# Kernel tuning notes

Hardware: AMD Instinct MI355X
Metric: run time of the kernel (lower is better)

The kernel has to match this reference:

```python
import jax, jax.numpy as jnp
import numpy as np

B_, T_, D_ = 4, 4096, 512
H_, DH_ = 8, 64
N_HASHES, BUCKET = 4, 64
SELF_ATTN_VAL = -5e4  # TOKEN_SELF_ATTN_VALUE from reformer-pytorch


def setup_inputs() -> dict:
    key = jax.random.key(0)
    ks = jax.random.split(key, 12)
    s = 0.02
    return {
        "src": jax.random.normal(ks[0], (B_, T_, D_), jnp.float32),
        "Wqk": jax.random.normal(ks[1], (D_, D_), jnp.float32) * s,
        "Wv": jax.random.normal(ks[2], (D_, D_), jnp.float32) * s,
        "Wout": jax.random.normal(ks[3], (D_, D_), jnp.float32) * s,
        "bout": jnp.zeros((D_,), jnp.float32),
        "W1": jax.random.normal(ks[4], (D_, 2048), jnp.float32) * s,
        "b1": jnp.zeros((2048,), jnp.float32),
        "W2": jax.random.normal(ks[5], (2048, D_), jnp.float32) * s,
        "b2": jnp.zeros((D_,), jnp.float32),
        "gamma": jnp.ones((D_,), jnp.float32),
        "beta": jnp.zeros((D_,), jnp.float32),
        "rotations": jax.random.normal(ks[6], (DH_, N_HASHES, (T_ // BUCKET) // 2), jnp.float32),
    }


def _look_one_back(x):
    # concat each chunk with the previous chunk (wraparound), along the slot axis
    prev = jnp.concatenate([x[:, -1:], x[:, :-1]], axis=1)
    return jnp.concatenate([x, prev], axis=2)


def lsh_attention(qk, v, rotations):
    # qk, v: (B, T, d) with B = batch*heads; shared-QK LSH attention (non-causal,
    # attend_across_buckets=True, allow_duplicate_attention=True, no dropout)
    B, T, d = qk.shape
    n_buckets = T // BUCKET
    # --- hashing ---
    rv = jnp.einsum("btf,fhi->bhti", qk, rotations)          # (B, n_hashes, T, nb/2)
    rv = jnp.concatenate([rv, -rv], axis=-1)                  # (B, n_hashes, T, nb)
    buckets = jnp.argmax(rv, axis=-1)                         # (B, n_hashes, T)
    offsets = (jnp.arange(N_HASHES) * n_buckets)[None, :, None]
    buckets = (buckets + offsets).reshape(B, N_HASHES * T)
    # --- sort by (bucket, position) ---
    ticker = jnp.arange(N_HASHES * T)
    buckets_and_t = buckets * T + (ticker % T)[None, :]
    sticker = jnp.argsort(buckets_and_t, axis=-1)             # (B, n_hashes*T)
    undo_sort = jnp.argsort(sticker, axis=-1)
    st = sticker % T
    sqk = jnp.take_along_axis(qk, st[..., None], axis=1)      # (B, n_hashes*T, d)
    sv = jnp.take_along_axis(v, st[..., None], axis=1)
    # --- chunk ---
    chunks = N_HASHES * n_buckets
    bq_t = st.reshape(B, chunks, BUCKET)
    bqk = sqk.reshape(B, chunks, BUCKET, d)
    bv = sv.reshape(B, chunks, BUCKET, d)
    bq = bqk
    bk = bqk / (jnp.linalg.norm(bqk, axis=-1, keepdims=True) + 1e-6)
    bk = _look_one_back(bk)                                   # (B, chunks, 2*BUCKET, d)
    bv = _look_one_back(bv)
    bkv_t = _look_one_back(bq_t)                              # (B, chunks, 2*BUCKET)
    # --- attention within chunk (+ one look-back chunk) ---
    dots = jnp.einsum("bcie,bcje->bcij", bq, bk) * (d ** -0.5)
    self_mask = bq_t[:, :, :, None] == bkv_t[:, :, None, :]
    dots = jnp.where(self_mask, SELF_ATTN_VAL, dots)
    lse = jax.nn.logsumexp(dots, axis=-1, keepdims=True)
    p = jnp.exp(dots - lse)
    bo = jnp.einsum("bcij,bcje->bcie", p, bv)
    # --- unsort and combine hash rounds ---
    so = bo.reshape(B, N_HASHES * T, d)
    slog = lse.reshape(B, N_HASHES * T)
    o = jnp.take_along_axis(so, undo_sort[..., None], axis=1)
    logits = jnp.take_along_axis(slog, undo_sort, axis=1)
    o = o.reshape(B, N_HASHES, T, d)
    logits = logits.reshape(B, N_HASHES, T, 1)
    probs = jnp.exp(logits - jax.nn.logsumexp(logits, axis=1, keepdims=True))
    return jnp.sum(o * probs, axis=1)                         # (B, T, d)


def _layer(src, Wqk, Wv, Wout, bout, W1, b1, W2, b2, gamma, beta, rotations):
    b, t, dm = src.shape
    qk = src @ Wqk
    v = src @ Wv
    def split(x):
        return x.reshape(b, t, H_, DH_).transpose(0, 2, 1, 3).reshape(b * H_, t, DH_)
    o = lsh_attention(split(qk), split(v), rotations)
    o = o.reshape(b, H_, t, DH_).transpose(0, 2, 1, 3).reshape(b, t, dm)
    attn_out = o @ Wout + bout
    x = src + attn_out                # residual (dropout = identity in eval)
    ffn = jax.nn.relu(x @ W1 + b1) @ W2 + b2
    y = x + ffn
    mu = jnp.mean(y, axis=-1, keepdims=True)
    var = jnp.mean((y - mu) ** 2, axis=-1, keepdims=True)
    return (y - mu) / jnp.sqrt(var + 1e-6) * gamma + beta     # post-norm (norm2)


def reference(src, Wqk, Wv, Wout, bout, W1, b1, W2, b2, gamma, beta, rotations):
    return _layer(src, Wqk, Wv, Wout, bout, W1, b1, W2, b2, gamma, beta, rotations)
```

## Files before the change

### kernel.cpp

```cpp
#include <hip/hip_runtime.h>

#define B_ 4
#define T_ 4096
#define D_ 512
#define H_ 8
#define DH_ 64
#define NH_ 4
#define NB_ 64
#define BH_ (B_*H_)
#define CHUNKS_ (NH_*NB_)
#define NTICK_ (NH_*T_)
#define M_ (B_*T_)
#define FFN_ 2048

typedef __attribute__((ext_vector_type(8))) short bf16x8;
typedef __attribute__((ext_vector_type(4))) float f32x4;

__device__ __forceinline__ unsigned short f2bf(float x) {
  unsigned int u = __float_as_uint(x);
  return (unsigned short)((u + 0x7FFFu + ((u >> 16) & 1u)) >> 16);
}
__device__ __forceinline__ float bf2f(unsigned short s) {
  return __uint_as_float(((unsigned int)s) << 16);
}

__device__ __forceinline__ void gld_lds16(const void* g, void* l) {
  __builtin_amdgcn_global_load_lds(
      (const __attribute__((address_space(1))) unsigned int*)g,
      (__attribute__((address_space(3))) unsigned int*)l, 16, 0, 0);
}

__device__ __forceinline__ int off64(int row, int k) {
  return row * 64 + (((k >> 3) ^ (row & 7)) << 3) + (k & 7);
}
__device__ __forceinline__ int off128(int row, int k) {
  return row * 128 + (((k >> 3) ^ (row & 7)) << 3) + (k & 7);
}

template<int OUT_MODE, bool HAS_BIAS, bool RELU, bool HAS_RESID, bool FUSE_INV>
__global__ __launch_bounds__(256) void gemm_bf16(
    const unsigned short* __restrict__ A, const unsigned short* __restrict__ BT,
    const float* __restrict__ bias, const unsigned short* __restrict__ resid,
    float* __restrict__ Cf, unsigned short* __restrict__ Cb,
    float* __restrict__ invn,
    int M, int N, int K, int lda, int ldbt, int ldr)
{
  __shared__ __align__(16) unsigned short smem[2 * 128 * 64];
  unsigned short* As = smem;
  unsigned short* Bs = smem + 128 * 64;
  const int tid = threadIdx.x;
  const int lane = tid & 63;
  const int w = tid >> 6;
  const int wm = (w >> 1) * 64, wn = (w & 1) * 64;
  const int g = lane >> 4, cl = lane & 15;
  const int m0 = blockIdx.y * 128, n0 = blockIdx.x * 128;

  f32x4 acc[4][4];
#pragma unroll
  for (int i = 0; i < 4; ++i)
#pragma unroll
    for (int j = 0; j < 4; ++j) acc[i][j] = (f32x4){0.f, 0.f, 0.f, 0.f};

  const int srow = tid >> 3;
  const int skc  = (tid & 7) * 8;

  for (int k0 = 0; k0 < K; k0 += 64) {
#pragma unroll
    for (int ci = 0; ci < 4; ++ci) {
      const int row = ci * 32 + srow;
      gld_lds16(&A [(size_t)(m0 + row) * lda  + k0 + skc], &As[ci * 2048 + tid * 8]);
      gld_lds16(&BT[(size_t)(n0 + row) * ldbt + k0 + skc], &Bs[ci * 2048 + tid * 8]);
    }
    __syncthreads();
#pragma unroll
    for (int kk = 0; kk < 64; kk += 32) {
      bf16x8 af[4], bfr[4];
#pragma unroll
      for (int i = 0; i < 4; ++i)
        af[i] = *(const bf16x8*)&As[(wm + i * 16 + cl) * 64 + kk + g * 8];
#pragma unroll
      for (int j = 0; j < 4; ++j)
        bfr[j] = *(const bf16x8*)&Bs[(wn + j * 16 + cl) * 64 + kk + g * 8];
#pragma unroll
      for (int i = 0; i < 4; ++i)
#pragma unroll
        for (int j = 0; j < 4; ++j)
          acc[i][j] = __builtin_amdgcn_mfma_f32_16x16x32_bf16(af[i], bfr[j], acc[i][j], 0, 0, 0);
    }
    __syncthreads();
  }

  float bv[4];
  if constexpr (HAS_BIAS) {
#pragma unroll
    for (int j = 0; j < 4; ++j) bv[j] = bias[n0 + wn + j * 16 + cl];
  }
#pragma unroll
  for (int i = 0; i < 4; ++i) {
#pragma unroll
    for (int r = 0; r < 4; ++r) {
      const int lrow = wm + i * 16 + g * 4 + r;
      float ss = 0.f;
#pragma unroll
      for (int j = 0; j < 4; ++j) {
        const int lcol = wn + j * 16 + cl;
        float val = acc[i][j][r];
        if constexpr (HAS_BIAS) val += bv[j];
        if constexpr (RELU) val = fmaxf(val, 0.f);
        if constexpr (FUSE_INV) ss += val * val;
        if constexpr (OUT_MODE == 2) Cf[(size_t)(m0 + lrow) * N + n0 + lcol] = val;
        smem[lrow * 128 + (lcol ^ ((lrow & 7) << 3))] = f2bf(val);
      }
      if constexpr (FUSE_INV) {
        ss += __shfl_xor(ss, 1); ss += __shfl_xor(ss, 2);
        ss += __shfl_xor(ss, 4); ss += __shfl_xor(ss, 8);
        if (cl == 0) {
          const int m = m0 + lrow;
          const int bb = m >> 12, t = m & (T_ - 1);
          const int hh = ((n0 + wn) >> 6) & 7;
          invn[((size_t)(bb * 8 + hh)) * T_ + t] = 1.0f / (sqrtf(ss) + 1e-6f);
        }
      }
    }
  }
  __syncthreads();
#pragma unroll
  for (int l = 0; l < 8; ++l) {
    const int idx = tid + l * 256;
    const int row = idx >> 4, c8 = (idx & 15) * 8;
    uint4 u = *(const uint4*)&smem[row * 128 + (c8 ^ ((row & 7) << 3))];
    if constexpr (HAS_RESID) {
      const uint4 rv = *(const uint4*)&resid[(size_t)(m0 + row) * ldr + n0 + c8];
      unsigned short* sp = (unsigned short*)&u;
      const unsigned short* rp = (const unsigned short*)&rv;
#pragma unroll
      for (int e = 0; e < 8; ++e) sp[e] = f2bf(bf2f(sp[e]) + bf2f(rp[e]));
    }
    *(uint4*)&Cb[(size_t)(m0 + row) * N + n0 + c8] = u;
  }
}

__global__ __launch_bounds__(256) void split_pair_kernel(
    const float* __restrict__ in, unsigned short* __restrict__ outp, int n8, int Dd)
{
  const int i = blockIdx.x * 256 + threadIdx.x;
  if (i >= n8) return;
  const int gpr = Dd >> 3;
  const int m = i / gpr, d0 = (i - m * gpr) * 8;
  float x[8];
  *(float4*)&x[0] = *(const float4*)&in[(size_t)m * Dd + d0];
  *(float4*)&x[4] = *(const float4*)&in[(size_t)m * Dd + d0 + 4];
  unsigned short hi[8], lo[8];
#pragma unroll
  for (int e = 0; e < 8; ++e) {
    hi[e] = f2bf(x[e]);
    lo[e] = f2bf(x[e] - bf2f(hi[e]));
  }
  *(uint4*)&outp[(size_t)m * 2 * Dd + d0]      = *(const uint4*)&hi[0];
  *(uint4*)&outp[(size_t)m * 2 * Dd + Dd + d0] = *(const uint4*)&lo[0];
}

__global__ __launch_bounds__(256) void prep_weights(
    const float* __restrict__ Wqk, const float* __restrict__ Wv,
    const float* __restrict__ Wout, const float* __restrict__ W1,
    const float* __restrict__ W2,
    unsigned short* __restrict__ WqkTp, unsigned short* __restrict__ WvT,
    unsigned short* __restrict__ WoutT, unsigned short* __restrict__ W1T,
    unsigned short* __restrict__ W2T)
{
  __shared__ float tile[32][33];
  int bid = blockIdx.x;
  const float* W; unsigned short* WT; int K, N, bx, by; bool split = false;
  if (bid < 256)        { W = Wqk;  WT = WqkTp; K = 512;  N = 512;  split = true;
                          bx = bid & 15; by = bid >> 4; }
  else if (bid < 512)   { bid -= 256;  W = Wv;   WT = WvT;   K = 512;  N = 512;
                          bx = bid & 15; by = bid >> 4; }
  else if (bid < 768)   { bid -= 512;  W = Wout; WT = WoutT; K = 512;  N = 512;
                          bx = bid & 15; by = bid >> 4; }
  else if (bid < 1792)  { bid -= 768;  W = W1;   WT = W1T;   K = 512;  N = 2048;
                          bx = bid & 63; by = bid >> 6; }
  else                  { bid -= 1792; W = W2;   WT = W2T;   K = 2048; N = 512;
                          bx = bid & 15; by = bid >> 4; }
  const int k0 = by * 32, n0 = bx * 32;
  const int tx = threadIdx.x & 31, ty = threadIdx.x >> 5;
#pragma unroll
  for (int r = 0; r < 32; r += 8)
    tile[ty + r][tx] = W[(size_t)(k0 + ty + r) * N + n0 + tx];
  __syncthreads();
  const int ld = split ? 2 * K : K;
#pragma unroll
  for (int r = 0; r < 32; r += 8) {
    const float x = tile[tx][ty + r];
    const unsigned short hi = f2bf(x);
    WT[(size_t)(n0 + ty + r) * ld + k0 + tx] = hi;
    if (split)
      WT[(size_t)(n0 + ty + r) * ld + K + k0 + tx] = f2bf(x - bf2f(hi));
  }
}

__global__ __launch_bounds__(256) void hash_gemm_kernel(
    const float* __restrict__ qk, const float* __restrict__ rot,
    int* __restrict__ buckets)
{
  __shared__ __align__(16) float As[64][136];
  __shared__ __align__(16) float Bs[64][132];
  const int tid = threadIdx.x;
  const int tx = tid & 15, ty = tid >> 4;
  const int t0 = blockIdx.x * 128, bh = blockIdx.y;
  const int b = bh >> 3, hd = bh & 7;

#pragma unroll
  for (int l = 0; l < 8; ++l) {
    const int idx = tid + l * 256;
    const int row = idx >> 4;
    const int kq = (idx & 15) << 2;
    const float4 a = *(const float4*)&qk[((size_t)b * T_ + t0 + row) * D_ + hd * DH_ + kq];
    As[kq + 0][row] = a.x; As[kq + 1][row] = a.y;
    As[kq + 2][row] = a.z; As[kq + 3][row] = a.w;
  }
#pragma unroll
  for (int l = 0; l < 8; ++l) {
    const int idx = tid + l * 256;
    const int kr = idx >> 5;
    const int c4 = (idx & 31) << 2;
    *(float4*)&Bs[kr][c4] = *(const float4*)&rot[kr * 128 + c4];
  }
  __syncthreads();

  float acc[8][8];
#pragma unroll
  for (int i = 0; i < 8; ++i)
#pragma unroll
    for (int j = 0; j < 8; ++j) acc[i][j] = 0.f;

#pragma unroll 4
  for (int kk = 0; kk < 64; ++kk) {
    float a[8], bq[8];
    *(float4*)&a[0]  = *(const float4*)&As[kk][ty * 8];
    *(float4*)&a[4]  = *(const float4*)&As[kk][ty * 8 + 4];
    *(float4*)&bq[0] = *(const float4*)&Bs[kk][tx * 8];
    *(float4*)&bq[4] = *(const float4*)&Bs[kk][tx * 8 + 4];
#pragma unroll
    for (int i = 0; i < 8; ++i)
#pragma unroll
      for (int j = 0; j < 8; ++j)
        acc[i][j] = fmaf(a[i], bq[j], acc[i][j]);
  }
  __syncthreads();

  float* pval = &As[0][0];
  int*   pidx = (int*)&Bs[0][0];
  const int i0 = (tx & 3) * 8;
#pragma unroll
  for (int r = 0; r < 8; ++r) {
    float v = -3.0e38f; int idx = 127;
#pragma unroll
    for (int j = 0; j < 8; ++j) {
      const float p = acc[r][j];
      const int li = i0 + j;
      if (p > v || (p == v && li < idx)) { v = p; idx = li; }
      const float n = -p;
      const int ni = 32 + li;
      if (n > v || (n == v && ni < idx)) { v = n; idx = ni; }
    }
    pval[(ty * 8 + r) * 16 + tx] = v;
    pidx[(ty * 8 + r) * 16 + tx] = idx;
  }
  __syncthreads();

#pragma unroll
  for (int l = 0; l < 2; ++l) {
    const int id = tid + l * 256;
    const int tok = id >> 2, hh = id & 3;
    float v = pval[tok * 16 + hh * 4];
    int idx = pidx[tok * 16 + hh * 4];
#pragma unroll
    for (int e = 1; e < 4; ++e) {
      const float ov = pval[tok * 16 + hh * 4 + e];
      const int oi = pidx[tok * 16 + hh * 4 + e];
      if (ov > v || (ov == v && oi < idx)) { v = ov; idx = oi; }
    }
    buckets[((size_t)bh * NH_ + hh) * T_ + t0 + tok] = idx + hh * NB_;
  }
}

__global__ __launch_bounds__(256) void hist_kernel(
    const int* __restrict__ buckets, int* __restrict__ bstart)
{
  __shared__ int bins[256];
  const int bh = blockIdx.x;
  bins[threadIdx.x] = 0;
  __syncthreads();
  for (int e = threadIdx.x; e < NTICK_; e += 256)
    atomicAdd(&bins[buckets[(size_t)bh * NTICK_ + e]], 1);
  __syncthreads();
  if (threadIdx.x == 0) {
    int run = 0;
    for (int i = 0; i < 256; ++i) { const int c = bins[i]; bins[i] = run; run += c; }
  }
  __syncthreads();
  bstart[bh * 256 + threadIdx.x] = bins[threadIdx.x];
}

__global__ __launch_bounds__(64) void compact_kernel(
    const int* __restrict__ buckets, const int* __restrict__ bstart,
    int* __restrict__ sticker)
{
  const int bucket = blockIdx.x, bh = blockIdx.y;
  const int h = bucket >> 6;
  const int lane = threadIdx.x;
  int base = bstart[bh * 256 + bucket];
  const int* bk = buckets + (size_t)bh * NTICK_ + (size_t)h * T_;
  for (int it = 0; it < 64; ++it) {
    const int t = it * 64 + lane;
    const bool m = (bk[t] == bucket);
    const unsigned long long bal = __ballot(m);
    if (m) {
      const int pos = base + __popcll(bal & ((1ull << lane) - 1ull));
      sticker[(size_t)bh * NTICK_ + pos] = h * T_ + t;
    }
    base += __popcll(bal);
  }
}

__global__ __launch_bounds__(256) void attn_kernel(
    const unsigned short* __restrict__ qkb, const unsigned short* __restrict__ vb,
    const int* __restrict__ sticker, const float* __restrict__ invn,
    unsigned short* __restrict__ orowsb, float* __restrict__ logits)
{
  __shared__ __align__(16) unsigned short Rs[128 * 64];
  __shared__ __align__(16) unsigned short Vs[128 * 64];
  __shared__ int tks[128];
  __shared__ float invs[128];

  const int c = blockIdx.x, bh = blockIdx.y;
  const int b = bh >> 3, hd = bh & 7;
  const int tid = threadIdx.x;
  const int hr = c >> 6;
  const int w = tid >> 6, lane = tid & 63, g = lane >> 4, cl = lane & 15;

  if (tid < 128) {
    const int sc = (tid < 64) ? c : ((c + CHUNKS_ - 1) & (CHUNKS_ - 1));
    const int tick = sticker[(size_t)bh * NTICK_ + sc * 64 + (tid & 63)];
    const int t = tick & (T_ - 1);
    tks[tid] = t;
    invs[tid] = invn[bh * T_ + t];
  }
  __syncthreads();

#pragma unroll
  for (int l = 0; l < 4; ++l) {
    const int idx = tid + l * 256;
    const int row = idx >> 3, k0 = (idx & 7) * 8;
    const size_t gb = ((size_t)b * T_ + tks[row]) * D_ + hd * DH_ + k0;
    *(uint4*)&Rs[off64(row, k0)] = *(const uint4*)&qkb[gb];
    *(uint4*)&Vs[off64(row, k0)] = *(const uint4*)&vb[gb];
  }
  __syncthreads();

  f32x4 sacc[8];
#pragma unroll
  for (int j = 0; j < 8; ++j) sacc[j] = (f32x4){0.f, 0.f, 0.f, 0.f};
#pragma unroll
  for (int kk = 0; kk < 2; ++kk) {
    const bf16x8 aq = *(const bf16x8*)&Rs[off64(w * 16 + cl, kk * 32 + g * 8)];
#pragma unroll
    for (int j = 0; j < 8; ++j) {
      const bf16x8 bk = *(const bf16x8*)&Rs[off64(j * 16 + cl, kk * 32 + g * 8)];
      sacc[j] = __builtin_amdgcn_mfma_f32_16x16x32_bf16(aq, bk, sacc[j], 0, 0, 0);
    }
  }
  unsigned short tr[4][8];
#pragma unroll
  for (int q = 0; q < 4; ++q) {
    const int gi = tid + q * 256;
    const int d = gi & 63, tg = gi >> 6;
#pragma unroll
    for (int e = 0; e < 8; ++e) tr[q][e] = Vs[off64(tg * 8 + e, d)];
  }
  __syncthreads();

#pragma unroll
  for (int q = 0; q < 4; ++q) {
    const int gi = tid + q * 256;
    const int d = gi & 63, tg = gi >> 6;
    *(uint4*)&Vs[off128(d, tg * 8)] = *(const uint4*)&tr[q][0];
  }

  float iv[8]; int tk[8];
#pragma unroll
  for (int j = 0; j < 8; ++j) {
    iv[j] = invs[j * 16 + cl] * 0.125f;
    tk[j] = tks[j * 16 + cl];
  }
  float pinv[4];
#pragma unroll
  for (int r = 0; r < 4; ++r) {
    const int row = w * 16 + g * 4 + r;
    const int tq = tks[row];
    float s[8];
    float mx = -3.0e38f;
#pragma unroll
    for (int j = 0; j < 8; ++j) {
      float d = sacc[j][r] * iv[j];
      if (tq == tk[j]) d = -5.0e4f;
      s[j] = d;
      mx = fmaxf(mx, d);
    }
    mx = fmaxf(mx, __shfl_xor(mx, 1)); mx = fmaxf(mx, __shfl_xor(mx, 2));
    mx = fmaxf(mx, __shfl_xor(mx, 4)); mx = fmaxf(mx, __shfl_xor(mx, 8));
    float sum = 0.f;
#pragma unroll
    for (int j = 0; j < 8; ++j) { s[j] = __expf(s[j] - mx); sum += s[j]; }
    sum += __shfl_xor(sum, 1); sum += __shfl_xor(sum, 2);
    sum += __shfl_xor(sum, 4); sum += __shfl_xor(sum, 8);
    pinv[r] = 1.f / sum;
#pragma unroll
    for (int j = 0; j < 8; ++j)
      Rs[off128(row, j * 16 + cl)] = f2bf(s[j]);
    if (cl == 0)
      logits[((size_t)bh * NH_ + hr) * T_ + tq] = mx + __logf(sum);
  }
  __syncthreads();

  f32x4 oacc[4];
#pragma unroll
  for (int jd = 0; jd < 4; ++jd) oacc[jd] = (f32x4){0.f, 0.f, 0.f, 0.f};
#pragma unroll
  for (int ks = 0; ks < 4; ++ks) {
    const bf16x8 pa = *(const bf16x8*)&Rs[off128(w * 16 + cl, ks * 32 + g * 8)];
#pragma unroll
    for (int jd = 0; jd < 4; ++jd) {
      const bf16x8 vv = *(const bf16x8*)&Vs[off128(jd * 16 + cl, ks * 32 + g * 8)];
      oacc[jd] = __builtin_amdgcn_mfma_f32_16x16x32_bf16(pa, vv, oacc[jd], 0, 0, 0);
    }
  }
  __syncthreads();

#pragma unroll
  for (int jd = 0; jd < 4; ++jd)
#pragma unroll
    for (int r = 0; r < 4; ++r)
      Rs[off64(w * 16 + g * 4 + r, jd * 16 + cl)] = f2bf(oacc[jd][r] * pinv[r]);
  __syncthreads();

#pragma unroll
  for (int l = 0; l < 2; ++l) {
    const int idx = tid + l * 256;
    const int row = idx >> 3, k0 = (idx & 7) * 8;
    *(uint4*)&orowsb[(((size_t)bh * NH_ + hr) * T_ + tks[row]) * DH_ + k0] =
        *(const uint4*)&Rs[off64(row, k0)];
  }
}

__global__ __launch_bounds__(256) void combine_kernel(
    const unsigned short* __restrict__ orowsb, const float* __restrict__ logits,
    unsigned short* __restrict__ ocombb)
{
  const int gid = blockIdx.x * 4 + (threadIdx.x >> 6);
  const int lane = threadIdx.x & 63;
  const int bh = gid >> 12, t = gid & (T_ - 1);
  const int b = bh >> 3, hd = bh & 7;
  const size_t lb = (size_t)bh * NH_ * T_ + t;
  const float l0 = logits[lb];
  const float l1 = logits[lb + T_];
  const float l2 = logits[lb + 2 * T_];
  const float l3 = logits[lb + 3 * T_];
  const float m = fmaxf(fmaxf(l0, l1), fmaxf(l2, l3));
  const float w0 = __expf(l0 - m), w1 = __expf(l1 - m);
  const float w2 = __expf(l2 - m), w3 = __expf(l3 - m);
  const float inv = 1.f / (w0 + w1 + w2 + w3);
  const size_t rb = ((size_t)bh * NH_ * T_ + t) * DH_ + lane;
  const size_t step = (size_t)T_ * DH_;
  const float o = w0 * bf2f(orowsb[rb]) + w1 * bf2f(orowsb[rb + step])
                + w2 * bf2f(orowsb[rb + 2 * step]) + w3 * bf2f(orowsb[rb + 3 * step]);
  ocombb[((size_t)b * T_ + t) * D_ + hd * DH_ + lane] = f2bf(o * inv);
}

__global__ __launch_bounds__(256) void ln_kernel(
    const unsigned short* __restrict__ yb, const float* __restrict__ gamma,
    const float* __restrict__ beta, float* __restrict__ out)
{
  const int row = blockIdx.x * 4 + (threadIdx.x >> 6);
  const int lane = threadIdx.x & 63;
  const size_t base = (size_t)row * D_ + lane * 8;
  const uint4 u = *(const uint4*)&yb[base];
  const unsigned short* up = (const unsigned short*)&u;
  float x[8];
#pragma unroll
  for (int i = 0; i < 8; ++i) x[i] = bf2f(up[i]);
  float s = 0.f;
#pragma unroll
  for (int i = 0; i < 8; ++i) s += x[i];
#pragma unroll
  for (int m = 32; m >= 1; m >>= 1) s += __shfl_xor(s, m);
  const float mu = s * (1.f / D_);
  float vs = 0.f;
#pragma unroll
  for (int i = 0; i < 8; ++i) { const float d = x[i] - mu; vs += d * d; }
#pragma unroll
  for (int m = 32; m >= 1; m >>= 1) vs += __shfl_xor(vs, m);
  const float rstd = rsqrtf(vs * (1.f / D_) + 1e-6f);
  float gm[8], bt[8];
  *(float4*)&gm[0] = *(const float4*)&gamma[lane * 8];
  *(float4*)&gm[4] = *(const float4*)&gamma[lane * 8 + 4];
  *(float4*)&bt[0] = *(const float4*)&beta[lane * 8];
  *(float4*)&bt[4] = *(const float4*)&beta[lane * 8 + 4];
  float o[8];
#pragma unroll
  for (int i = 0; i < 8; ++i) o[i] = (x[i] - mu) * rstd * gm[i] + bt[i];
  *(float4*)&out[base]     = make_float4(o[0], o[1], o[2], o[3]);
  *(float4*)&out[base + 4] = make_float4(o[4], o[5], o[6], o[7]);
}

extern "C" void kernel_launch(void* const* d_in, const int* in_sizes, int n_in,
                              void* d_out, int out_size, void* d_ws, size_t ws_size,
                              hipStream_t stream) {
  (void)in_sizes; (void)n_in; (void)out_size; (void)ws_size;
  const float* src   = (const float*)d_in[0];
  const float* Wqk   = (const float*)d_in[1];
  const float* Wv    = (const float*)d_in[2];
  const float* Wout  = (const float*)d_in[3];
  const float* bout  = (const float*)d_in[4];
  const float* W1    = (const float*)d_in[5];
  const float* b1    = (const float*)d_in[6];
  const float* W2    = (const float*)d_in[7];
  const float* b2    = (const float*)d_in[8];
  const float* gamma = (const float*)d_in[9];
  const float* beta  = (const float*)d_in[10];
  const float* rot   = (const float*)d_in[11];
  float* out = (float*)d_out;

  char* ws = (char*)d_ws;
  const size_t MB = 1024 * 1024;
  float*          qk       = (float*)(ws);
  unsigned short* src_pair = (unsigned short*)(ws + 32 * MB);
  unsigned short* v_b      = (unsigned short*)(ws + 64 * MB);
  unsigned short* orows_b  = (unsigned short*)(ws + 80 * MB);
  unsigned short* qk_b     = (unsigned short*)(ws + 144 * MB);
  char* p = ws + 160 * MB;
  float* logits  = (float*)p; p += (size_t)BH_ * NH_ * T_ * 4;
  int*   buckets = (int*)p;   p += (size_t)BH_ * NH_ * T_ * 4;
  int*   sticker = (int*)p;   p += (size_t)BH_ * NTICK_ * 4;
  int*   bstart  = (int*)p;   p += (size_t)BH_ * 256 * 4;
  float* invn    = (float*)p; p += (size_t)BH_ * T_ * 4;
  unsigned short* WvT    = (unsigned short*)p; p += (size_t)D_ * D_ * 2;
  unsigned short* WoutT  = (unsigned short*)p; p += (size_t)D_ * D_ * 2;
  unsigned short* W1T    = (unsigned short*)p; p += (size_t)FFN_ * D_ * 2;
  unsigned short* W2T    = (unsigned short*)p; p += (size_t)D_ * FFN_ * 2;
  unsigned short* WqkTp  = (unsigned short*)p; p += (size_t)D_ * 2 * D_ * 2;

  unsigned short* ocomb_b  = qk_b;
  unsigned short* x_b      = v_b;
  unsigned short* hidden_b = orows_b;
  unsigned short* ybuf_b   = (unsigned short*)ws;

  prep_weights<<<2816, 256, 0, stream>>>(Wqk, Wv, Wout, W1, W2,
                                         WqkTp, WvT, WoutT, W1T, W2T);
  split_pair_kernel<<<M_ * D_ / 8 / 256, 256, 0, stream>>>(src, src_pair, M_ * D_ / 8, D_);

  gemm_bf16<2, false, false, false, true><<<dim3(D_ / 128, M_ / 128), 256, 0, stream>>>(
      src_pair, WqkTp, nullptr, nullptr, qk, qk_b, invn, M_, D_, 2 * D_, 2 * D_, 2 * D_, 0);
  gemm_bf16<1, false, false, false, false><<<dim3(D_ / 128, M_ / 128), 256, 0, stream>>>(
      src_pair, WvT, nullptr, nullptr, nullptr, v_b, nullptr, M_, D_, D_, 2 * D_, D_, 0);
  hash_gemm_kernel<<<dim3(T_ / 128, BH_), 256, 0, stream>>>(qk, rot, buckets);
  hist_kernel<<<BH_, 256, 0, stream>>>(buckets, bstart);
  compact_kernel<<<dim3(256, BH_), 64, 0, stream>>>(buckets, bstart, sticker);
  attn_kernel<<<dim3(CHUNKS_, BH_), 256, 0, stream>>>(
      qk_b, v_b, sticker, invn, orows_b, logits);
  combine_kernel<<<BH_ * T_ / 4, 256, 0, stream>>>(orows_b, logits, ocomb_b);
  gemm_bf16<1, true, false, true, false><<<dim3(D_ / 128, M_ / 128), 256, 0, stream>>>(
      ocomb_b, WoutT, bout, src_pair, nullptr, x_b, nullptr, M_, D_, D_, D_, D_, 2 * D_);
  gemm_bf16<1, true, true, false, false><<<dim3(FFN_ / 128, M_ / 128), 256, 0, stream>>>(
      x_b, W1T, b1, nullptr, nullptr, hidden_b, nullptr, M_, FFN_, D_, D_, D_, 0);
  gemm_bf16<1, true, false, true, false><<<dim3(D_ / 128, M_ / 128), 256, 0, stream>>>(
      hidden_b, W2T, b2, x_b, nullptr, ybuf_b, nullptr, M_, D_, FFN_, FFN_, FFN_, D_);
  ln_kernel<<<M_ / 4, 256, 0, stream>>>(ybuf_b, gamma, beta, out);
}
```

Measured before the change: 388.0 us.

## Swizzle block order, merge prep kernels, drop softmax max, interleave hash outputs

Remaps GEMM and attention block indices with an 8-way XCD-style swizzle, so neighbouring tiles share L2 on the same die. Merges the weight-transpose and src split kernels into one launch. Removes the per-row max subtraction in the attention softmax, which risks overflow if logits are large. Stores logits and per-hash outputs interleaved by token so the combine step reads them contiguously, and rewrites the V transpose to use wider LDS reads.

Result: faster. 366.2 us (-5.6%).

```diff
diff --git a/kernel.cpp b/kernel.cpp
--- a/kernel.cpp
+++ b/kernel.cpp
@@ -53,7 +53,12 @@
   const int w = tid >> 6;
   const int wm = (w >> 1) * 64, wn = (w & 1) * 64;
   const int g = lane >> 4, cl = lane & 15;
-  const int m0 = blockIdx.y * 128, n0 = blockIdx.x * 128;
+
+  const int gx = gridDim.x;
+  const int id = blockIdx.x + blockIdx.y * gx;
+  const int cpx = (gx * gridDim.y) >> 3;
+  const int swz = (id & 7) * cpx + (id >> 3);
+  const int m0 = (swz / gx) * 128, n0 = (swz % gx) * 128;
 
   f32x4 acc[4][4];
 #pragma unroll
@@ -140,36 +145,33 @@
   }
 }
 
-__global__ __launch_bounds__(256) void split_pair_kernel(
-    const float* __restrict__ in, unsigned short* __restrict__ outp, int n8, int Dd)
-{
-  const int i = blockIdx.x * 256 + threadIdx.x;
-  if (i >= n8) return;
-  const int gpr = Dd >> 3;
-  const int m = i / gpr, d0 = (i - m * gpr) * 8;
-  float x[8];
-  *(float4*)&x[0] = *(const float4*)&in[(size_t)m * Dd + d0];
-  *(float4*)&x[4] = *(const float4*)&in[(size_t)m * Dd + d0 + 4];
-  unsigned short hi[8], lo[8];
-#pragma unroll
-  for (int e = 0; e < 8; ++e) {
-    hi[e] = f2bf(x[e]);
-    lo[e] = f2bf(x[e] - bf2f(hi[e]));
-  }
-  *(uint4*)&outp[(size_t)m * 2 * Dd + d0]      = *(const uint4*)&hi[0];
-  *(uint4*)&outp[(size_t)m * 2 * Dd + Dd + d0] = *(const uint4*)&lo[0];
-}
-
-__global__ __launch_bounds__(256) void prep_weights(
+__global__ __launch_bounds__(256) void prep_all(
     const float* __restrict__ Wqk, const float* __restrict__ Wv,
     const float* __restrict__ Wout, const float* __restrict__ W1,
-    const float* __restrict__ W2,
+    const float* __restrict__ W2, const float* __restrict__ src,
     unsigned short* __restrict__ WqkTp, unsigned short* __restrict__ WvT,
     unsigned short* __restrict__ WoutT, unsigned short* __restrict__ W1T,
-    unsigned short* __restrict__ W2T)
+    unsigned short* __restrict__ W2T, unsigned short* __restrict__ src_pair)
 {
   __shared__ float tile[32][33];
   int bid = blockIdx.x;
+  if (bid >= 2816) {
+    const int i = (bid - 2816) * 256 + threadIdx.x;
+    const int gpr = D_ >> 3;
+    const int m = i / gpr, d0 = (i - m * gpr) * 8;
+    float x[8];
+    *(float4*)&x[0] = *(const float4*)&src[(size_t)m * D_ + d0];
+    *(float4*)&x[4] = *(const float4*)&src[(size_t)m * D_ + d0 + 4];
+    unsigned short hi[8], lo[8];
+#pragma unroll
+    for (int e = 0; e < 8; ++e) {
+      hi[e] = f2bf(x[e]);
+      lo[e] = f2bf(x[e] - bf2f(hi[e]));
+    }
+    *(uint4*)&src_pair[(size_t)m * 2 * D_ + d0]      = *(const uint4*)&hi[0];
+    *(uint4*)&src_pair[(size_t)m * 2 * D_ + D_ + d0] = *(const uint4*)&lo[0];
+    return;
+  }
   const float* W; unsigned short* WT; int K, N, bx, by; bool split = false;
   if (bid < 256)        { W = Wqk;  WT = WqkTp; K = 512;  N = 512;  split = true;
                           bx = bid & 15; by = bid >> 4; }
@@ -333,7 +335,9 @@
   __shared__ int tks[128];
   __shared__ float invs[128];
 
-  const int c = blockIdx.x, bh = blockIdx.y;
+  const int cx = blockIdx.x;
+  const int c = (cx & 7) * 32 + (cx >> 3);
+  const int bh = blockIdx.y;
   const int b = bh >> 3, hd = bh & 7;
   const int tid = threadIdx.x;
   const int hr = c >> 6;
@@ -370,21 +374,27 @@
       sacc[j] = __builtin_amdgcn_mfma_f32_16x16x32_bf16(aq, bk, sacc[j], 0, 0, 0);
     }
   }
-  unsigned short tr[4][8];
-#pragma unroll
-  for (int q = 0; q < 4; ++q) {
-    const int gi = tid + q * 256;
-    const int d = gi & 63, tg = gi >> 6;
-#pragma unroll
-    for (int e = 0; e < 8; ++e) tr[q][e] = Vs[off64(tg * 8 + e, d)];
-  }
-  __syncthreads();
-
-#pragma unroll
-  for (int q = 0; q < 4; ++q) {
-    const int gi = tid + q * 256;
-    const int d = gi & 63, tg = gi >> 6;
-    *(uint4*)&Vs[off128(d, tg * 8)] = *(const uint4*)&tr[q][0];
+  const int d0 = (tid & 15) * 4, tg = tid >> 4;
+  unsigned int qw[8][2];
+#pragma unroll
+  for (int e = 0; e < 8; ++e) {
+    const uint2 q = *(const uint2*)&Vs[off64(tg * 8 + e, d0)];
+    qw[e][0] = q.x; qw[e][1] = q.y;
+  }
+  __syncthreads();
+
+  {
+    unsigned short col[4][8];
+#pragma unroll
+    for (int e = 0; e < 8; ++e) {
+      col[0][e] = (unsigned short)(qw[e][0] & 0xffffu);
+      col[1][e] = (unsigned short)(qw[e][0] >> 16);
+      col[2][e] = (unsigned short)(qw[e][1] & 0xffffu);
+      col[3][e] = (unsigned short)(qw[e][1] >> 16);
+    }
+#pragma unroll
+    for (int dd = 0; dd < 4; ++dd)
+      *(uint4*)&Vs[off128(d0 + dd, tg * 8)] = *(const uint4*)&col[dd][0];
   }
 
   float iv[8]; int tk[8];
@@ -398,28 +408,23 @@
   for (int r = 0; r < 4; ++r) {
     const int row = w * 16 + g * 4 + r;
     const int tq = tks[row];
-    float s[8];
-    float mx = -3.0e38f;
+    float e8[8];
+    float sum = 0.f;
 #pragma unroll
     for (int j = 0; j < 8; ++j) {
-      float d = sacc[j][r] * iv[j];
-      if (tq == tk[j]) d = -5.0e4f;
-      s[j] = d;
-      mx = fmaxf(mx, d);
-    }
-    mx = fmaxf(mx, __shfl_xor(mx, 1)); mx = fmaxf(mx, __shfl_xor(mx, 2));
-    mx = fmaxf(mx, __shfl_xor(mx, 4)); mx = fmaxf(mx, __shfl_xor(mx, 8));
-    float sum = 0.f;
-#pragma unroll
-    for (int j = 0; j < 8; ++j) { s[j] = __expf(s[j] - mx); sum += s[j]; }
+      float e = __expf(sacc[j][r] * iv[j]);
+      if (tq == tk[j]) e = 0.f;
+      e8[j] = e;
+      sum += e;
+    }
     sum += __shfl_xor(sum, 1); sum += __shfl_xor(sum, 2);
     sum += __shfl_xor(sum, 4); sum += __shfl_xor(sum, 8);
     pinv[r] = 1.f / sum;
 #pragma unroll
     for (int j = 0; j < 8; ++j)
-      Rs[off128(row, j * 16 + cl)] = f2bf(s[j]);
+      Rs[off128(row, j * 16 + cl)] = f2bf(e8[j]);
     if (cl == 0)
-      logits[((size_t)bh * NH_ + hr) * T_ + tq] = mx + __logf(sum);
+      logits[((size_t)bh * T_ + tq) * NH_ + hr] = __logf(sum);
   }
   __syncthreads();
 
@@ -448,7 +453,7 @@
   for (int l = 0; l < 2; ++l) {
     const int idx = tid + l * 256;
     const int row = idx >> 3, k0 = (idx & 7) * 8;
-    *(uint4*)&orowsb[(((size_t)bh * NH_ + hr) * T_ + tks[row]) * DH_ + k0] =
+    *(uint4*)&orowsb[(((size_t)bh * T_ + tks[row]) * NH_ + hr) * DH_ + k0] =
         *(const uint4*)&Rs[off64(row, k0)];
   }
 }
@@ -461,19 +466,16 @@
   const int lane = threadIdx.x & 63;
   const int bh = gid >> 12, t = gid & (T_ - 1);
   const int b = bh >> 3, hd = bh & 7;
-  const size_t lb = (size_t)bh * NH_ * T_ + t;
-  const float l0 = logits[lb];
-  const float l1 = logits[lb + T_];
-  const float l2 = logits[lb + 2 * T_];
-  const float l3 = logits[lb + 3 * T_];
-  const float m = fmaxf(fmaxf(l0, l1), fmaxf(l2, l3));
-  const float w0 = __expf(l0 - m), w1 = __expf(l1 - m);
-  const float w2 = __expf(l2 - m), w3 = __expf(l3 - m);
+  const float4 lg = *(const float4*)&logits[((size_t)bh * T_ + t) * NH_];
+  const float m = fmaxf(fmaxf(lg.x, lg.y), fmaxf(lg.z, lg.w));
+  const float w0 = __expf(lg.x - m), w1 = __expf(lg.y - m);
+  const float w2 = __expf(lg.z - m), w3 = __expf(lg.w - m);
   const float inv = 1.f / (w0 + w1 + w2 + w3);
-  const size_t rb = ((size_t)bh * NH_ * T_ + t) * DH_ + lane;
-  const size_t step = (size_t)T_ * DH_;
-  const float o = w0 * bf2f(orowsb[rb]) + w1 * bf2f(orowsb[rb + step])
-                + w2 * bf2f(orowsb[rb + 2 * step]) + w3 * bf2f(orowsb[rb + 3 * step]);
+  const size_t rb = ((size_t)bh * T_ + t) * (NH_ * DH_) + lane;
+  const float o = w0 * bf2f(orowsb[rb])
+                + w1 * bf2f(orowsb[rb + DH_])
+                + w2 * bf2f(orowsb[rb + 2 * DH_])
+                + w3 * bf2f(orowsb[rb + 3 * DH_]);
   ocombb[((size_t)b * T_ + t) * D_ + hd * DH_ + lane] = f2bf(o * inv);
 }
 
@@ -555,9 +557,8 @@
   unsigned short* hidden_b = orows_b;
   unsigned short* ybuf_b   = (unsigned short*)ws;
 
-  prep_weights<<<2816, 256, 0, stream>>>(Wqk, Wv, Wout, W1, W2,
-                                         WqkTp, WvT, WoutT, W1T, W2T);
-  split_pair_kernel<<<M_ * D_ / 8 / 256, 256, 0, stream>>>(src, src_pair, M_ * D_ / 8, D_);
+  prep_all<<<2816 + M_ * D_ / 8 / 256, 256, 0, stream>>>(
+      Wqk, Wv, Wout, W1, W2, src, WqkTp, WvT, WoutT, W1T, W2T, src_pair);
 
   gemm_bf16<2, false, false, false, true><<<dim3(D_ / 128, M_ / 128), 256, 0, stream>>>(
       src_pair, WqkTp, nullptr, nullptr, qk, qk_b, invn, M_, D_, 2 * D_, 2 * D_, 2 * D_, 0);
```
